# Kernel tuning notes

Hardware: AMD Instinct MI355X
Metric: run time of the kernel (lower is better)

## Reference

```python
import jax, jax.numpy as jnp
import numpy as np

B, N, F, O = 2, 8192, 64, 64

def setup_inputs() -> dict:
    key = jax.random.key(0)
    k1, k2, k3, k4, k5 = jax.random.split(key, 5)
    x = jax.random.normal(k1, (B, N, F), dtype=jnp.float32)
    adj_w = jax.random.normal(k2, (2 * F,), dtype=jnp.float32) * (1.0 / np.sqrt(2 * F))
    adj_b = jax.random.normal(k3, (1,), dtype=jnp.float32)
    weight = jax.random.normal(k4, (F, O), dtype=jnp.float32) * (1.0 / np.sqrt(F))
    bias = jax.random.normal(k5, (O,), dtype=jnp.float32)
    return {"x": x, "adj_w": adj_w, "adj_b": adj_b, "weight": weight, "bias": bias}

def reference(x, adj_w, adj_b, weight, bias):
    # Original: tmp[b,i,j]=x[b,j]; cat(tmp, tmp.T) -> [x[b,j], x[b,i]] -> Linear(2F,1).
    # Algebraically separable: adj[b,i,j] = w_j . x[b,j] + w_i . x[b,i] + b
    Fdim = x.shape[-1]
    w_j, w_i = adj_w[:Fdim], adj_w[Fdim:]
    sj = jnp.einsum('bnf,f->bn', x, w_j)  # contribution of column node j
    si = jnp.einsum('bnf,f->bn', x, w_i)  # contribution of row node i
    adj = si[:, :, None] + sj[:, None, :] + adj_b[0]  # (B,N,N)
    out = jnp.einsum('bnf,fo->bno', x, weight)  # (B,N,O)
    deg_inv_sqrt = jnp.maximum(adj.sum(axis=-1), 1.0) ** -0.5  # clamp(min=1).pow(-0.5)
    adj = deg_inv_sqrt[:, :, None] * adj * deg_inv_sqrt[:, None, :]
    out = jnp.einsum('bij,bjo->bio', adj, out) + bias
    return jax.nn.relu(out)
```

## Files before the change

### kernel.cpp

```cpp
#include <hip/hip_runtime.h>


#define NN 8192
#define FF 64

__global__ __launch_bounds__(256) void k1_sisj(const float* __restrict__ x,
                                               const float* __restrict__ adj_w,
                                               float* __restrict__ si,
                                               float* __restrict__ sj,
                                               float* __restrict__ parts1) {
    __shared__ float wjs[FF], wis[FF], sjs[64];
    int tid = threadIdx.x;
    if (tid < 2 * FF) {
        float v = adj_w[tid];
        if (tid < FF) wjs[tid] = v; else wis[tid - FF] = v;
    }
    __syncthreads();
    int q4 = tid & 15, rl = tid >> 4;
    float4 wjv = reinterpret_cast<const float4*>(wjs)[q4];
    float4 wiv = reinterpret_cast<const float4*>(wis)[q4];
    int rowbase = blockIdx.x * 64;
    #pragma unroll
    for (int pass = 0; pass < 4; ++pass) {
        int r = pass * 16 + rl;
        int row = rowbase + r;
        float4 xv = reinterpret_cast<const float4*>(x + (size_t)row * FF)[q4];
        float a = xv.x * wjv.x + xv.y * wjv.y + xv.z * wjv.z + xv.w * wjv.w;
        float b = xv.x * wiv.x + xv.y * wiv.y + xv.z * wiv.z + xv.w * wiv.w;
        #pragma unroll
        for (int s = 8; s; s >>= 1) {
            a += __shfl_down(a, s, 16);
            b += __shfl_down(b, s, 16);
        }
        if (q4 == 0) { sj[row] = a; si[row] = b; sjs[r] = a; }
    }
    __syncthreads();
    if (tid < 64) {
        float a = sjs[tid];
        #pragma unroll
        for (int s = 32; s; s >>= 1) a += __shfl_down(a, s, 64);
        if (tid == 0) parts1[blockIdx.x] = a;
    }
}

__global__ __launch_bounds__(256) void k2_pq(const float* __restrict__ x,
                                             const float* __restrict__ adj_b,
                                             const float* __restrict__ si,
                                             const float* __restrict__ sj,
                                             const float* __restrict__ parts1,
                                             float* __restrict__ dglob,
                                             float* __restrict__ p2,
                                             float* __restrict__ q2) {
    __shared__ float red[128], dsh[128], sjdsh[128];
    __shared__ float pacc[256], qacc[256];
    __shared__ float SjTs;
    int tid = threadIdx.x;
    int batch = blockIdx.x >> 6;
    int base = batch * NN + (blockIdx.x & 63) * 128;
    if (tid < 128) red[tid] = parts1[batch * 128 + tid];
    __syncthreads();
    if (tid < 64) {
        float a = red[tid] + red[tid + 64];
        #pragma unroll
        for (int s = 32; s; s >>= 1) a += __shfl_down(a, s, 64);
        if (tid == 0) SjTs = a;
    }
    __syncthreads();
    float cadj = adj_b[0];
    if (tid < 128) {
        int row = base + tid;
        float siv = si[row], sjv = sj[row];
        float d = rsqrtf(fmaxf(8192.f * (siv + cadj) + SjTs, 1.f));
        dsh[tid] = d; sjdsh[tid] = sjv * d;
        dglob[row] = d;
    }
    __syncthreads();
    int f = tid & 63, g = tid >> 6;
    float pa = 0.f, qa = 0.f;
    for (int r = g; r < 128; r += 4) {
        float xv = x[(size_t)(base + r) * FF + f];
        pa += dsh[r] * xv;
        qa += sjdsh[r] * xv;
    }
    pacc[tid] = pa; qacc[tid] = qa;
    __syncthreads();
    if (tid < 64) {
        p2[blockIdx.x * 64 + tid] = pacc[tid] + pacc[tid + 64] + pacc[tid + 128] + pacc[tid + 192];
        q2[blockIdx.x * 64 + tid] = qacc[tid] + qacc[tid + 64] + qacc[tid + 128] + qacc[tid + 192];
    }
}

__global__ __launch_bounds__(256) void k3_out(const float* __restrict__ adj_b,
                                              const float* __restrict__ weight,
                                              const float* __restrict__ bias,
                                              const float* __restrict__ si,
                                              const float* __restrict__ dglob,
                                              const float* __restrict__ p2,
                                              const float* __restrict__ q2,
                                              float* __restrict__ out) {
    __shared__ float pacc[256], qacc[256];
    __shared__ float ps[64], qs[64], Us[64], Vs[64];
    __shared__ float dr[64], sir[64];
    int tid = threadIdx.x;
    int batch = blockIdx.x >> 7;
    int rowbase = blockIdx.x * 64;
    if (tid < 64) { dr[tid] = dglob[rowbase + tid]; sir[tid] = si[rowbase + tid]; }
    int f = tid & 63, g = tid >> 6;
    float pa = 0.f, qa = 0.f;
    for (int b2 = g; b2 < 64; b2 += 4) {
        size_t idx = (size_t)(batch * 64 + b2) * 64 + f;
        pa += p2[idx];
        qa += q2[idx];
    }
    pacc[tid] = pa; qacc[tid] = qa;
    __syncthreads();
    if (tid < 64) {
        ps[tid] = pacc[tid] + pacc[tid + 64] + pacc[tid + 128] + pacc[tid + 192];
        qs[tid] = qacc[tid] + qacc[tid + 64] + qacc[tid + 128] + qacc[tid + 192];
    }
    __syncthreads();
    if (tid < 128) {
        int sel = tid >> 6, o = tid & 63;
        const float* src = sel ? qs : ps;
        float s = 0.f;
        #pragma unroll
        for (int k = 0; k < FF; ++k) s += src[k] * weight[k * 64 + o];
        (sel ? Vs : Us)[o] = s;
    }
    __syncthreads();
    float cadj = adj_b[0];
    int q4 = tid & 15, rl = tid >> 4;
    float4 bv = reinterpret_cast<const float4*>(bias)[q4];
    float4 Uv = reinterpret_cast<const float4*>(Us)[q4];
    float4 Vv = reinterpret_cast<const float4*>(Vs)[q4];
    #pragma unroll
    for (int pass = 0; pass < 4; ++pass) {
        int r = pass * 16 + rl;
        int row = rowbase + r;
        float d = dr[r];
        float a = d * (sir[r] + cadj);
        float4 o;
        o.x = fmaxf(a * Uv.x + d * Vv.x + bv.x, 0.f);
        o.y = fmaxf(a * Uv.y + d * Vv.y + bv.y, 0.f);
        o.z = fmaxf(a * Uv.z + d * Vv.z + bv.z, 0.f);
        o.w = fmaxf(a * Uv.w + d * Vv.w + bv.w, 0.f);
        reinterpret_cast<float4*>(out + (size_t)row * FF)[q4] = o;
    }
}

extern "C" void kernel_launch(void* const* d_in, const int* in_sizes, int n_in,
                              void* d_out, int out_size, void* d_ws, size_t ws_size,
                              hipStream_t stream) {
    const float* x      = (const float*)d_in[0];
    const float* adj_w  = (const float*)d_in[1];
    const float* adj_b  = (const float*)d_in[2];
    const float* weight = (const float*)d_in[3];
    const float* bias   = (const float*)d_in[4];
    float* out = (float*)d_out;

    float* ws     = (float*)d_ws;
    float* si     = ws;
    float* sj     = ws + 16384;
    float* dglob  = ws + 32768;
    float* parts1 = ws + 49152;
    float* p2     = ws + 49408;
    float* q2     = ws + 57600;

    k1_sisj<<<256, 256, 0, stream>>>(x, adj_w, si, sj, parts1);
    k2_pq  <<<128, 256, 0, stream>>>(x, adj_b, si, sj, parts1, dglob, p2, q2);
    k3_out <<<256, 256, 0, stream>>>(adj_b, weight, bias, si, dglob, p2, q2, out);
}
```

Measured before the change: 81.08 us.

## Fuse three GCN kernels into one persistent kernel with grid-wide atomic barriers

Merges the three kernels into a single launch of 256 blocks. The blocks synchronise per batch through atomic counters and spin-waits. Each block keeps its x tile, si, sj and d values in shared memory, so x is read from global memory once and the intermediate arrays are no longer written out. The cost removed is the launch gaps between kernels and the extra global traffic. In exchange it adds a memset, spin barriers that depend on all blocks being resident at once, and a float atomicAdd for the column sum whose result is not deterministic.

```diff
diff --git a/kernel.cpp b/kernel.cpp
--- a/kernel.cpp
+++ b/kernel.cpp
@@ -4,27 +4,44 @@
 #define NN 8192
 #define FF 64
 
-__global__ __launch_bounds__(256) void k1_sisj(const float* __restrict__ x,
-                                               const float* __restrict__ adj_w,
-                                               float* __restrict__ si,
-                                               float* __restrict__ sj,
-                                               float* __restrict__ parts1) {
-    __shared__ float wjs[FF], wis[FF], sjs[64];
-    int tid = threadIdx.x;
+__global__ __launch_bounds__(256) void fused_gcn(
+    const float* __restrict__ x,
+    const float* __restrict__ adj_w,
+    const float* __restrict__ adj_b,
+    const float* __restrict__ weight,
+    const float* __restrict__ bias,
+    float* __restrict__ p2,
+    float* __restrict__ q2,
+    unsigned int* __restrict__ cnt,
+    float* __restrict__ sjt_acc,
+    float* __restrict__ out)
+{
+    __shared__ float wjs[FF], wis[FF];
+    __shared__ float xs[64 * FF];
+    __shared__ float sish[64], sjsh[64], dsh[64], sjdsh[64];
+    __shared__ float pacc[256], qacc[256];
+    __shared__ float ps[64], qs[64], Us[64], Vs[64];
+    __shared__ float SjTs;
+
+    const int tid = threadIdx.x;
+    const int bid = blockIdx.x;
+    const int batch = bid >> 7;
+    const int rowbase = bid * 64;
+
     if (tid < 2 * FF) {
         float v = adj_w[tid];
         if (tid < FF) wjs[tid] = v; else wis[tid - FF] = v;
     }
     __syncthreads();
-    int q4 = tid & 15, rl = tid >> 4;
+
+    const int q4 = tid & 15, rl = tid >> 4;
     float4 wjv = reinterpret_cast<const float4*>(wjs)[q4];
     float4 wiv = reinterpret_cast<const float4*>(wis)[q4];
-    int rowbase = blockIdx.x * 64;
     #pragma unroll
     for (int pass = 0; pass < 4; ++pass) {
         int r = pass * 16 + rl;
-        int row = rowbase + r;
-        float4 xv = reinterpret_cast<const float4*>(x + (size_t)row * FF)[q4];
+        float4 xv = reinterpret_cast<const float4*>(x + (size_t)(rowbase + r) * FF)[q4];
+        reinterpret_cast<float4*>(xs)[r * 16 + q4] = xv;
         float a = xv.x * wjv.x + xv.y * wjv.y + xv.z * wjv.z + xv.w * wjv.w;
         float b = xv.x * wiv.x + xv.y * wiv.y + xv.z * wiv.z + xv.w * wiv.w;
         #pragma unroll
@@ -32,87 +49,74 @@
             a += __shfl_down(a, s, 16);
             b += __shfl_down(b, s, 16);
         }
-        if (q4 == 0) { sj[row] = a; si[row] = b; sjs[r] = a; }
+        if (q4 == 0) { sjsh[r] = a; sish[r] = b; }
     }
     __syncthreads();
     if (tid < 64) {
-        float a = sjs[tid];
+        float a = sjsh[tid];
         #pragma unroll
         for (int s = 32; s; s >>= 1) a += __shfl_down(a, s, 64);
-        if (tid == 0) parts1[blockIdx.x] = a;
+        if (tid == 0) atomicAdd(&sjt_acc[batch], a);
     }
-}
 
-__global__ __launch_bounds__(256) void k2_pq(const float* __restrict__ x,
-                                             const float* __restrict__ adj_b,
-                                             const float* __restrict__ si,
-                                             const float* __restrict__ sj,
-                                             const float* __restrict__ parts1,
-                                             float* __restrict__ dglob,
-                                             float* __restrict__ p2,
-                                             float* __restrict__ q2) {
-    __shared__ float red[128], dsh[128], sjdsh[128];
-    __shared__ float pacc[256], qacc[256];
-    __shared__ float SjTs;
-    int tid = threadIdx.x;
-    int batch = blockIdx.x >> 6;
-    int base = batch * NN + (blockIdx.x & 63) * 128;
-    if (tid < 128) red[tid] = parts1[batch * 128 + tid];
+    __syncthreads();
+    if (tid == 0) {
+        __threadfence();
+        atomicAdd(&cnt[batch], 1u);
+        while (__hip_atomic_load(&cnt[batch], __ATOMIC_RELAXED,
+                                 __HIP_MEMORY_SCOPE_AGENT) < 128u)
+            __builtin_amdgcn_s_sleep(2);
+        __threadfence();
+        SjTs = __hip_atomic_load(&sjt_acc[batch], __ATOMIC_RELAXED,
+                                 __HIP_MEMORY_SCOPE_AGENT);
+    }
+    __syncthreads();
+
+    float cadj = adj_b[0];
+    if (tid < 64) {
+        float d = rsqrtf(fmaxf(8192.f * (sish[tid] + cadj) + SjTs, 1.f));
+        dsh[tid] = d;
+        sjdsh[tid] = sjsh[tid] * d;
+    }
+    __syncthreads();
+    const int f = tid & 63, g = tid >> 6;
+    {
+        float pa = 0.f, qa = 0.f;
+        #pragma unroll
+        for (int r = g; r < 64; r += 4) {
+            float xv = xs[r * FF + f];
+            pa += dsh[r] * xv;
+            qa += sjdsh[r] * xv;
+        }
+        pacc[tid] = pa; qacc[tid] = qa;
+    }
     __syncthreads();
     if (tid < 64) {
-        float a = red[tid] + red[tid + 64];
-        #pragma unroll
-        for (int s = 32; s; s >>= 1) a += __shfl_down(a, s, 64);
-        if (tid == 0) SjTs = a;
+        p2[bid * 64 + tid] = pacc[tid] + pacc[tid + 64] + pacc[tid + 128] + pacc[tid + 192];
+        q2[bid * 64 + tid] = qacc[tid] + qacc[tid + 64] + qacc[tid + 128] + qacc[tid + 192];
+    }
+
+    __syncthreads();
+    if (tid == 0) {
+        __threadfence();
+        atomicAdd(&cnt[2 + batch], 1u);
+        while (__hip_atomic_load(&cnt[2 + batch], __ATOMIC_RELAXED,
+                                 __HIP_MEMORY_SCOPE_AGENT) < 128u)
+            __builtin_amdgcn_s_sleep(2);
+        __threadfence();
     }
     __syncthreads();
-    float cadj = adj_b[0];
-    if (tid < 128) {
-        int row = base + tid;
-        float siv = si[row], sjv = sj[row];
-        float d = rsqrtf(fmaxf(8192.f * (siv + cadj) + SjTs, 1.f));
-        dsh[tid] = d; sjdsh[tid] = sjv * d;
-        dglob[row] = d;
+
+    {
+        float pa = 0.f, qa = 0.f;
+        int base = batch * 128;
+        #pragma unroll 4
+        for (int b2 = g; b2 < 128; b2 += 4) {
+            pa += p2[(base + b2) * 64 + f];
+            qa += q2[(base + b2) * 64 + f];
+        }
+        pacc[tid] = pa; qacc[tid] = qa;
     }
-    __syncthreads();
-    int f = tid & 63, g = tid >> 6;
-    float pa = 0.f, qa = 0.f;
-    for (int r = g; r < 128; r += 4) {
-        float xv = x[(size_t)(base + r) * FF + f];
-        pa += dsh[r] * xv;
-        qa += sjdsh[r] * xv;
-    }
-    pacc[tid] = pa; qacc[tid] = qa;
-    __syncthreads();
-    if (tid < 64) {
-        p2[blockIdx.x * 64 + tid] = pacc[tid] + pacc[tid + 64] + pacc[tid + 128] + pacc[tid + 192];
-        q2[blockIdx.x * 64 + tid] = qacc[tid] + qacc[tid + 64] + qacc[tid + 128] + qacc[tid + 192];
-    }
-}
-
-__global__ __launch_bounds__(256) void k3_out(const float* __restrict__ adj_b,
-                                              const float* __restrict__ weight,
-                                              const float* __restrict__ bias,
-                                              const float* __restrict__ si,
-                                              const float* __restrict__ dglob,
-                                              const float* __restrict__ p2,
-                                              const float* __restrict__ q2,
-                                              float* __restrict__ out) {
-    __shared__ float pacc[256], qacc[256];
-    __shared__ float ps[64], qs[64], Us[64], Vs[64];
-    __shared__ float dr[64], sir[64];
-    int tid = threadIdx.x;
-    int batch = blockIdx.x >> 7;
-    int rowbase = blockIdx.x * 64;
-    if (tid < 64) { dr[tid] = dglob[rowbase + tid]; sir[tid] = si[rowbase + tid]; }
-    int f = tid & 63, g = tid >> 6;
-    float pa = 0.f, qa = 0.f;
-    for (int b2 = g; b2 < 64; b2 += 4) {
-        size_t idx = (size_t)(batch * 64 + b2) * 64 + f;
-        pa += p2[idx];
-        qa += q2[idx];
-    }
-    pacc[tid] = pa; qacc[tid] = qa;
     __syncthreads();
     if (tid < 64) {
         ps[tid] = pacc[tid] + pacc[tid + 64] + pacc[tid + 128] + pacc[tid + 192];
@@ -128,23 +132,21 @@
         (sel ? Vs : Us)[o] = s;
     }
     __syncthreads();
-    float cadj = adj_b[0];
-    int q4 = tid & 15, rl = tid >> 4;
+
     float4 bv = reinterpret_cast<const float4*>(bias)[q4];
     float4 Uv = reinterpret_cast<const float4*>(Us)[q4];
     float4 Vv = reinterpret_cast<const float4*>(Vs)[q4];
     #pragma unroll
     for (int pass = 0; pass < 4; ++pass) {
         int r = pass * 16 + rl;
-        int row = rowbase + r;
-        float d = dr[r];
-        float a = d * (sir[r] + cadj);
+        float d = dsh[r];
+        float a = d * (sish[r] + cadj);
         float4 o;
         o.x = fmaxf(a * Uv.x + d * Vv.x + bv.x, 0.f);
         o.y = fmaxf(a * Uv.y + d * Vv.y + bv.y, 0.f);
         o.z = fmaxf(a * Uv.z + d * Vv.z + bv.z, 0.f);
         o.w = fmaxf(a * Uv.w + d * Vv.w + bv.w, 0.f);
-        reinterpret_cast<float4*>(out + (size_t)row * FF)[q4] = o;
+        reinterpret_cast<float4*>(out + (size_t)(rowbase + r) * FF)[q4] = o;
     }
 }
 
@@ -158,15 +160,12 @@
     const float* bias   = (const float*)d_in[4];
     float* out = (float*)d_out;
 
-    float* ws     = (float*)d_ws;
-    float* si     = ws;
-    float* sj     = ws + 16384;
-    float* dglob  = ws + 32768;
-    float* parts1 = ws + 49152;
-    float* p2     = ws + 49408;
-    float* q2     = ws + 57600;
+    unsigned int* cnt = (unsigned int*)d_ws;
+    float* sjt_acc    = (float*)d_ws + 4;
+    float* p2         = (float*)d_ws + 8;
+    float* q2         = (float*)d_ws + 8 + 16384;
 
-    k1_sisj<<<256, 256, 0, stream>>>(x, adj_w, si, sj, parts1);
-    k2_pq  <<<128, 256, 0, stream>>>(x, adj_b, si, sj, parts1, dglob, p2, q2);
-    k3_out <<<256, 256, 0, stream>>>(adj_b, weight, bias, si, dglob, p2, q2, out);
+    hipMemsetAsync(d_ws, 0, 24, stream);
+    fused_gcn<<<256, 256, 0, stream>>>(x, adj_w, adj_b, weight, bias,
+                                       p2, q2, cnt, sjt_acc, out);
 }
```

Result: slower. 110.8 us (+36.6%).
